# Kernel tuning notes

Hardware: AMD Instinct MI355X
Metric: run time of the kernel (lower is better)

## Reference

```python
import jax, jax.numpy as jnp
import numpy as np

D, H, E = 1024, 4096, 8


def setup_inputs() -> dict:
    key = jax.random.key(0)
    ks = jax.random.split(key, 8)
    s_in = 1.0 / np.sqrt(D)
    s_hid = 1.0 / np.sqrt(H)
    return {
        "x": jax.random.normal(ks[0], (4, 2048, D), dtype=jnp.float32),
        # torch nn.Linear init ~ U(-1/sqrt(fan_in), 1/sqrt(fan_in)); exact dist irrelevant for a numeric reference
        "Wg": jax.random.uniform(ks[1], (D, E), jnp.float32, -s_in, s_in),
        "bg": jax.random.uniform(ks[2], (E,), jnp.float32, -s_in, s_in),
        "W1": jax.random.uniform(ks[3], (E, D, H), jnp.float32, -s_in, s_in),
        "b1": jax.random.uniform(ks[4], (E, H), jnp.float32, -s_in, s_in),
        "W2": jax.random.uniform(ks[5], (E, H, D), jnp.float32, -s_hid, s_hid),
        "b2": jax.random.uniform(ks[6], (E, D), jnp.float32, -s_hid, s_hid),
    }


def reference(x, Wg, bg, W1, b1, W2, b2):
    # gate
    gate_logits = jnp.einsum("bsd,de->bse", x, Wg) + bg
    gate_probs = jax.nn.softmax(gate_logits, axis=-1)
    expert_indices = jnp.argmax(gate_probs, axis=-1)  # [B,S]

    # Faithful to source: mask the INPUT per expert, run the full MLP on the
    # masked input (biases still apply to zeroed tokens!), and sum all experts.
    onehot = jax.nn.one_hot(expert_indices, E, dtype=x.dtype)  # [B,S,E]
    xm = jnp.einsum("bsd,bse->ebsd", x, onehot)                # [E,B,S,D]
    h = jax.nn.relu(jnp.einsum("ebsd,edh->ebsh", xm, W1) + b1[:, None, None, :])
    out_e = jnp.einsum("ebsh,ehd->ebsd", h, W2) + b2[:, None, None, :]
    combined_output = jnp.sum(out_e, axis=0)                   # [B,S,D]
    return combined_output, gate_probs, expert_indices
```

## Files before the change

### kernel.cpp

```cpp
#include <hip/hip_runtime.h>
#include <hip/hip_bf16.h>
#include <cstdint>

#define D_DIM 1024
#define H_DIM 4096
#define E_NUM 8
#define NTOK  8192

#define BM 128
#define BN 128
#define BK 32

#define MAXT 72
#define NBY1 (H_DIM / BN)
#define NBY2 (D_DIM / BN)

typedef __bf16 bf16;
typedef __bf16 bf16x8 __attribute__((ext_vector_type(8)));
typedef __bf16 bf16x4 __attribute__((ext_vector_type(4)));
typedef float  f32x4  __attribute__((ext_vector_type(4)));

#define GLOAD16(g, l)                                                          \
    __builtin_amdgcn_global_load_lds(                                          \
        (const __attribute__((address_space(1))) void*)(g),                    \
        (__attribute__((address_space(3))) void*)(l), 16, 0, 0)

__global__ __launch_bounds__(256) void gate_kernel(
    const float* __restrict__ x, const float* __restrict__ Wg,
    const float* __restrict__ bg, float* __restrict__ out_probs,
    float* __restrict__ out_idx, int* __restrict__ cnt, int* __restrict__ list)
{
    const int t = blockIdx.x * 4 + (threadIdx.x >> 6);
    const int l = threadIdx.x & 63;
    double part[E_NUM];
#pragma unroll
    for (int e = 0; e < E_NUM; e++) part[e] = 0.0;
    const float* xr = x + (size_t)t * D_DIM;
#pragma unroll
    for (int i = 0; i < D_DIM / 64; i++) {
        const int d = l + i * 64;
        const float xv = xr[d];
        const float* wr = Wg + (size_t)d * E_NUM;
        float4 w0 = *(const float4*)(wr);
        float4 w1 = *(const float4*)(wr + 4);
        part[0] += (double)xv * (double)w0.x;
        part[1] += (double)xv * (double)w0.y;
        part[2] += (double)xv * (double)w0.z;
        part[3] += (double)xv * (double)w0.w;
        part[4] += (double)xv * (double)w1.x;
        part[5] += (double)xv * (double)w1.y;
        part[6] += (double)xv * (double)w1.z;
        part[7] += (double)xv * (double)w1.w;
    }
#pragma unroll
    for (int e = 0; e < E_NUM; e++) {
        double v = part[e];
        for (int s = 32; s > 0; s >>= 1) v += __shfl_xor(v, s, 64);
        part[e] = v;
    }
    if (l == 0) {
        float logits[E_NUM], probs[E_NUM];
        float m = -3.0e38f;
#pragma unroll
        for (int e = 0; e < E_NUM; e++) {
            logits[e] = (float)(part[e] + (double)bg[e]);
            m = fmaxf(m, logits[e]);
        }
        float s = 0.f;
#pragma unroll
        for (int e = 0; e < E_NUM; e++) { probs[e] = expf(logits[e] - m); s += probs[e]; }
        const float inv = 1.f / s;
        int best = 0; float bp = -1.f;
#pragma unroll
        for (int e = 0; e < E_NUM; e++) {
            probs[e] *= inv;
            if (probs[e] > bp) { bp = probs[e]; best = e; }
        }
#pragma unroll
        for (int e = 0; e < E_NUM; e++) out_probs[(size_t)t * E_NUM + e] = probs[e];
        out_idx[t] = (float)best;
        const int pos = atomicAdd(&cnt[best], 1);
        list[best * NTOK + pos] = t;
    }
}

__global__ __launch_bounds__(256) void zero_kernel(int* cnt, float* cpartial)
{
    const int i = blockIdx.x * 256 + threadIdx.x;
    if (i < E_NUM * D_DIM) cpartial[i] = 0.f;
    if (i < E_NUM) cnt[i] = 0;
}

__global__ void offsets_kernel(const int* __restrict__ cnt, int* __restrict__ off,
                               int* __restrict__ tile_e, int* __restrict__ tile_row,
                               int* __restrict__ tile_n)
{
    if (threadIdx.x == 0) {
        int a = 0, n = 0;
        for (int e = 0; e < E_NUM; e++) {
            off[e] = a; a += cnt[e];
            for (int rr = 0; rr < cnt[e]; rr += BM) {
                tile_e[n] = e; tile_row[n] = rr; n++;
            }
        }
        tile_n[0] = n;
    }
}

__global__ __launch_bounds__(256) void gather_kernel(
    const float* __restrict__ x, const int* __restrict__ off,
    const int* __restrict__ cnt, const int* __restrict__ list,
    bf16* __restrict__ Xg)
{
    const int p = blockIdx.x;
    int e = 0;
    while (e < E_NUM - 1 && p >= off[e] + cnt[e]) e++;
    const int token = list[e * NTOK + (p - off[e])];
    const float* src = x + (size_t)token * D_DIM;
    bf16* dst = Xg + (size_t)p * D_DIM;
    const int t = threadIdx.x;
    float4 v = *(const float4*)(src + t * 4);
    bf16x4 o;
    o[0] = (bf16)v.x; o[1] = (bf16)v.y; o[2] = (bf16)v.z; o[3] = (bf16)v.w;
    *(bf16x4*)(dst + t * 4) = o;
}

__global__ __launch_bounds__(256) void transpose_conv_kernel(
    const float* __restrict__ in, bf16* __restrict__ out, int K, int N)
{
    const int e = blockIdx.z;
    const float* src = in + (size_t)e * K * N;
    bf16* dst = out + (size_t)e * K * N;
    __shared__ float T[64][65];
    const int t = threadIdx.x;
    const int k0 = blockIdx.x * 64, n0 = blockIdx.y * 64;
    {
        const int ty = t >> 4;
        const int tx = (t & 15) * 4;
#pragma unroll
        for (int i = 0; i < 4; i++) {
            f32x4 v = __builtin_nontemporal_load(
                (const f32x4*)(src + (size_t)(k0 + ty + 16 * i) * N + n0 + tx));
            T[ty + 16 * i][tx + 0] = v[0]; T[ty + 16 * i][tx + 1] = v[1];
            T[ty + 16 * i][tx + 2] = v[2]; T[ty + 16 * i][tx + 3] = v[3];
        }
    }
    __syncthreads();
    {
        const int n  = t >> 2;
        const int kx = (t & 3) * 16;
        bf16 tmp[16];
#pragma unroll
        for (int j = 0; j < 16; j++) tmp[j] = (bf16)T[kx + j][n];
        *(bf16x8*)(dst + (size_t)(n0 + n) * K + k0 + kx)     = *(bf16x8*)&tmp[0];
        *(bf16x8*)(dst + (size_t)(n0 + n) * K + k0 + kx + 8) = *(bf16x8*)&tmp[8];
    }
}

__global__ __launch_bounds__(256) void transpose_conv_w2_kernel(
    const float* __restrict__ in, const float* __restrict__ b1,
    bf16* __restrict__ out, float* __restrict__ cpartial)
{
    const int K = H_DIM, N = D_DIM;
    const int e = blockIdx.z;
    const float* src = in + (size_t)e * K * N;
    bf16* dst = out + (size_t)e * K * N;
    __shared__ float T[64][65];
    const int t = threadIdx.x;
    const int k0 = blockIdx.x * 64, n0 = blockIdx.y * 64;
    {
        const int ty = t >> 4;
        const int tx = (t & 15) * 4;
#pragma unroll
        for (int i = 0; i < 4; i++) {
            f32x4 v = __builtin_nontemporal_load(
                (const f32x4*)(src + (size_t)(k0 + ty + 16 * i) * N + n0 + tx));
            T[ty + 16 * i][tx + 0] = v[0]; T[ty + 16 * i][tx + 1] = v[1];
            T[ty + 16 * i][tx + 2] = v[2]; T[ty + 16 * i][tx + 3] = v[3];
        }
    }
    __syncthreads();
    {
        const int n  = t >> 2;
        const int kx = (t & 3) * 16;
        bf16 tmp[16];
#pragma unroll
        for (int j = 0; j < 16; j++) tmp[j] = (bf16)T[kx + j][n];
        *(bf16x8*)(dst + (size_t)(n0 + n) * K + k0 + kx)     = *(bf16x8*)&tmp[0];
        *(bf16x8*)(dst + (size_t)(n0 + n) * K + k0 + kx + 8) = *(bf16x8*)&tmp[8];
    }
    if (t < 64) {
        float s = 0.f;
#pragma unroll 8
        for (int h = 0; h < 64; h++)
            s += fmaxf(b1[(size_t)e * H_DIM + k0 + h], 0.f) * T[h][t];
        atomicAdd(&cpartial[(size_t)e * D_DIM + n0 + t], s);
    }
}

__global__ __launch_bounds__(256) void cfinal_kernel(
    const float* __restrict__ cpartial, const float* __restrict__ b2,
    float* __restrict__ adj)
{
    const int d = blockIdx.x * 256 + threadIdx.x;
    float c[E_NUM];
    float tot = 0.f;
#pragma unroll
    for (int e = 0; e < E_NUM; e++) {
        c[e] = cpartial[(size_t)e * D_DIM + d] + b2[(size_t)e * D_DIM + d];
        tot += c[e];
    }
#pragma unroll
    for (int e = 0; e < E_NUM; e++) adj[(size_t)e * D_DIM + d] = tot - c[e];
}

__global__ __launch_bounds__(256) void gemm1_kernel(
    const bf16* __restrict__ Xg, const bf16* __restrict__ W1t,
    const float* __restrict__ b1, const int* __restrict__ cnt,
    const int* __restrict__ off, const int* __restrict__ tile_e,
    const int* __restrict__ tile_row, const int* __restrict__ tile_n,
    bf16* __restrict__ Hb)
{
    const int orig = blockIdx.x;
    const int q = (MAXT * NBY1) >> 3;
    const int fid = (orig & 7) * q + (orig >> 3);
    const int tx = fid % MAXT;
    const int by = fid / MAXT;
    if (tx >= tile_n[0]) return;
    const int e  = tile_e[tx];
    const int m0 = tile_row[tx];
    const int ne = cnt[e];
    const int oe = off[e];

    __shared__ bf16 As[BM * BK];
    __shared__ bf16 Bs[BN * BK];

    const int t = threadIdx.x;
    const int w = t >> 6, lane = t & 63;
    const int wr = w >> 1, wc = w & 1;
    const int lrow = lane & 15, kq = (lane >> 4) * 8;

    const int lr = lane >> 2;
    const int lc = (lane & 3) * 8;
    const bf16* Ast = Xg + ((size_t)(oe + m0 + w * 32 + lr)) * D_DIM + lc;
    const bf16* Bst = W1t + ((size_t)e * H_DIM + by * BN + w * 32 + lr) * D_DIM + lc;
    bf16* Alds = As + (w * 32) * BK;
    bf16* Blds = Bs + (w * 32) * BK;

    f32x4 acc[4][4];
#pragma unroll
    for (int m = 0; m < 4; m++)
#pragma unroll
        for (int n = 0; n < 4; n++) acc[m][n] = (f32x4){0.f, 0.f, 0.f, 0.f};

    for (int kt = 0; kt < D_DIM / BK; kt++) {
        const int kc = kt * BK;
        GLOAD16(Ast + kc,              Alds);
        GLOAD16(Ast + 16 * D_DIM + kc, Alds + 16 * BK);
        GLOAD16(Bst + kc,              Blds);
        GLOAD16(Bst + 16 * D_DIM + kc, Blds + 16 * BK);
        __syncthreads();

        bf16x8 af[4], bfr[4];
#pragma unroll
        for (int m = 0; m < 4; m++)
            af[m] = *(const bf16x8*)&As[(wr * 64 + m * 16 + lrow) * BK + kq];
#pragma unroll
        for (int n = 0; n < 4; n++)
            bfr[n] = *(const bf16x8*)&Bs[(wc * 64 + n * 16 + lrow) * BK + kq];
#pragma unroll
        for (int m = 0; m < 4; m++)
#pragma unroll
            for (int n = 0; n < 4; n++)
                acc[m][n] = __builtin_amdgcn_mfma_f32_16x16x32_bf16(af[m], bfr[n], acc[m][n], 0, 0, 0);
        __syncthreads();
    }

#pragma unroll
    for (int m = 0; m < 4; m++) {
        const int rb0 = m0 + wr * 64 + m * 16 + ((lane >> 4) << 2);
#pragma unroll
        for (int n = 0; n < 4; n++) {
            const int gcol = by * BN + wc * 64 + n * 16 + (lane & 15);
            const float bias = b1[(size_t)e * H_DIM + gcol];
#pragma unroll
            for (int r = 0; r < 4; r++) {
                const int grow = rb0 + r;
                if (grow < ne) {
                    float v = acc[m][n][r] + bias;
                    Hb[((size_t)(oe + grow)) * H_DIM + gcol] = (bf16)fmaxf(v, 0.f);
                }
            }
        }
    }
}

__global__ __launch_bounds__(256) void gemm2_kernel(
    const bf16* __restrict__ Hb, const bf16* __restrict__ W2t,
    const float* __restrict__ b2, const float* __restrict__ adj,
    const int* __restrict__ cnt, const int* __restrict__ off,
    const int* __restrict__ tile_e, const int* __restrict__ tile_row,
    const int* __restrict__ tile_n, const int* __restrict__ list,
    float* __restrict__ out)
{
    const int orig = blockIdx.x;
    const int q = (MAXT * NBY2) >> 3;
    const int fid = (orig & 7) * q + (orig >> 3);
    const int tx = fid % MAXT;
    const int by = fid / MAXT;
    if (tx >= tile_n[0]) return;
    const int e  = tile_e[tx];
    const int m0 = tile_row[tx];
    const int ne = cnt[e];
    const int oe = off[e];

    __shared__ bf16 As[BM * BK];
    __shared__ bf16 Bs[BN * BK];

    const int t = threadIdx.x;
    const int w = t >> 6, lane = t & 63;
    const int wr = w >> 1, wc = w & 1;
    const int lrow = lane & 15, kq = (lane >> 4) * 8;

    const int lr = lane >> 2;
    const int lc = (lane & 3) * 8;
    const bf16* Ast = Hb + ((size_t)(oe + m0 + w * 32 + lr)) * H_DIM + lc;
    const bf16* Bst = W2t + ((size_t)e * D_DIM + by * BN + w * 32 + lr) * H_DIM + lc;
    bf16* Alds = As + (w * 32) * BK;
    bf16* Blds = Bs + (w * 32) * BK;

    f32x4 acc[4][4];
#pragma unroll
    for (int m = 0; m < 4; m++)
#pragma unroll
        for (int n = 0; n < 4; n++) acc[m][n] = (f32x4){0.f, 0.f, 0.f, 0.f};

    for (int kt = 0; kt < H_DIM / BK; kt++) {
        const int kc = kt * BK;
        GLOAD16(Ast + kc,              Alds);
        GLOAD16(Ast + 16 * H_DIM + kc, Alds + 16 * BK);
        GLOAD16(Bst + kc,              Blds);
        GLOAD16(Bst + 16 * H_DIM + kc, Blds + 16 * BK);
        __syncthreads();

        bf16x8 af[4], bfr[4];
#pragma unroll
        for (int m = 0; m < 4; m++)
            af[m] = *(const bf16x8*)&As[(wr * 64 + m * 16 + lrow) * BK + kq];
#pragma unroll
        for (int n = 0; n < 4; n++)
            bfr[n] = *(const bf16x8*)&Bs[(wc * 64 + n * 16 + lrow) * BK + kq];
#pragma unroll
        for (int m = 0; m < 4; m++)
#pragma unroll
            for (int n = 0; n < 4; n++)
                acc[m][n] = __builtin_amdgcn_mfma_f32_16x16x32_bf16(af[m], bfr[n], acc[m][n], 0, 0, 0);
        __syncthreads();
    }

#pragma unroll
    for (int m = 0; m < 4; m++) {
        const int rb0 = m0 + wr * 64 + m * 16 + ((lane >> 4) << 2);
#pragma unroll
        for (int n = 0; n < 4; n++) {
            const int gcol = by * BN + wc * 64 + n * 16 + (lane & 15);
            const float badj = b2[(size_t)e * D_DIM + gcol] + adj[(size_t)e * D_DIM + gcol];
#pragma unroll
            for (int r = 0; r < 4; r++) {
                const int grow = rb0 + r;
                if (grow < ne) {
                    const int tok = list[e * NTOK + grow];
                    out[(size_t)tok * D_DIM + gcol] = acc[m][n][r] + badj;
                }
            }
        }
    }
}

extern "C" void kernel_launch(void* const* d_in, const int* in_sizes, int n_in,
                              void* d_out, int out_size, void* d_ws, size_t ws_size,
                              hipStream_t stream)
{
    (void)in_sizes; (void)n_in; (void)out_size; (void)ws_size;
    const float* x  = (const float*)d_in[0];
    const float* Wg = (const float*)d_in[1];
    const float* bg = (const float*)d_in[2];
    const float* W1 = (const float*)d_in[3];
    const float* b1 = (const float*)d_in[4];
    const float* W2 = (const float*)d_in[5];
    const float* b2 = (const float*)d_in[6];

    float* out_comb  = (float*)d_out;
    float* out_probs = out_comb + (size_t)NTOK * D_DIM;
    float* out_idx   = out_probs + (size_t)NTOK * E_NUM;

    char* ws = (char*)d_ws;
    size_t o = 0;
    bf16* W1t = (bf16*)(ws + o); o += (size_t)E_NUM * H_DIM * D_DIM * 2;
    bf16* W2t = (bf16*)(ws + o); o += (size_t)E_NUM * H_DIM * D_DIM * 2;
    bf16* Hb  = (bf16*)(ws + o); o += (size_t)NTOK * H_DIM * 2;
    bf16* Xg  = (bf16*)(ws + o); o += (size_t)NTOK * D_DIM * 2;
    float* cpartial = (float*)(ws + o); o += (size_t)E_NUM * D_DIM * 4;
    float* adj      = (float*)(ws + o); o += (size_t)E_NUM * D_DIM * 4;
    int* cnt  = (int*)(ws + o); o += 256;
    int* off  = (int*)(ws + o); o += 256;
    int* tile_e   = (int*)(ws + o); o += 512;
    int* tile_row = (int*)(ws + o); o += 512;
    int* tile_n   = (int*)(ws + o); o += 256;
    int* list = (int*)(ws + o); o += (size_t)E_NUM * NTOK * 4;

    zero_kernel<<<(E_NUM * D_DIM + 255) / 256, 256, 0, stream>>>(cnt, cpartial);
    gate_kernel<<<NTOK / 4, 256, 0, stream>>>(x, Wg, bg, out_probs, out_idx, cnt, list);
    offsets_kernel<<<1, 64, 0, stream>>>(cnt, off, tile_e, tile_row, tile_n);
    gather_kernel<<<NTOK, 256, 0, stream>>>(x, off, cnt, list, Xg);
    transpose_conv_w2_kernel<<<dim3(H_DIM / 64, D_DIM / 64, E_NUM), 256, 0, stream>>>(W2, b1, W2t, cpartial);
    cfinal_kernel<<<D_DIM / 256, 256, 0, stream>>>(cpartial, b2, adj);
    transpose_conv_kernel<<<dim3(D_DIM / 64, H_DIM / 64, E_NUM), 256, 0, stream>>>(W1, W1t, D_DIM, H_DIM);
    gemm1_kernel<<<MAXT * NBY1, 256, 0, stream>>>(Xg, W1t, b1, cnt, off, tile_e, tile_row, tile_n, Hb);
    gemm2_kernel<<<MAXT * NBY2, 256, 0, stream>>>(Hb, W2t, b2, adj, cnt, off, tile_e, tile_row, tile_n, list, out_comb);
}
```

Baseline: 441.1 us.

## Split-K the second expert GEMM and add a reduction kernel

```diff
diff --git a/kernel.cpp b/kernel.cpp
--- a/kernel.cpp
+++ b/kernel.cpp
@@ -14,6 +14,8 @@
 #define MAXT 72
 #define NBY1 (H_DIM / BN)
 #define NBY2 (D_DIM / BN)
+#define KSPLIT 2
+#define KC_LEN (H_DIM / KSPLIT)
 
 typedef __bf16 bf16;
 typedef __bf16 bf16x8 __attribute__((ext_vector_type(8)));
@@ -297,17 +299,17 @@
 
 __global__ __launch_bounds__(256) void gemm2_kernel(
     const bf16* __restrict__ Hb, const bf16* __restrict__ W2t,
-    const float* __restrict__ b2, const float* __restrict__ adj,
     const int* __restrict__ cnt, const int* __restrict__ off,
     const int* __restrict__ tile_e, const int* __restrict__ tile_row,
-    const int* __restrict__ tile_n, const int* __restrict__ list,
-    float* __restrict__ out)
+    const int* __restrict__ tile_n, float* __restrict__ part)
 {
     const int orig = blockIdx.x;
-    const int q = (MAXT * NBY2) >> 3;
+    const int q = (MAXT * NBY2 * KSPLIT) >> 3;
     const int fid = (orig & 7) * q + (orig >> 3);
     const int tx = fid % MAXT;
-    const int by = fid / MAXT;
+    const int byk = fid / MAXT;
+    const int by = byk >> 1;
+    const int kcs = byk & 1;
     if (tx >= tile_n[0]) return;
     const int e  = tile_e[tx];
     const int m0 = tile_row[tx];
@@ -324,8 +326,9 @@
 
     const int lr = lane >> 2;
     const int lc = (lane & 3) * 8;
-    const bf16* Ast = Hb + ((size_t)(oe + m0 + w * 32 + lr)) * H_DIM + lc;
-    const bf16* Bst = W2t + ((size_t)e * D_DIM + by * BN + w * 32 + lr) * H_DIM + lc;
+    const size_t kbase = (size_t)kcs * KC_LEN;
+    const bf16* Ast = Hb + ((size_t)(oe + m0 + w * 32 + lr)) * H_DIM + kbase + lc;
+    const bf16* Bst = W2t + ((size_t)e * D_DIM + by * BN + w * 32 + lr) * H_DIM + kbase + lc;
     bf16* Alds = As + (w * 32) * BK;
     bf16* Blds = Bs + (w * 32) * BK;
 
@@ -335,7 +338,7 @@
 #pragma unroll
         for (int n = 0; n < 4; n++) acc[m][n] = (f32x4){0.f, 0.f, 0.f, 0.f};
 
-    for (int kt = 0; kt < H_DIM / BK; kt++) {
+    for (int kt = 0; kt < KC_LEN / BK; kt++) {
         const int kc = kt * BK;
         GLOAD16(Ast + kc,              Alds);
         GLOAD16(Ast + 16 * H_DIM + kc, Alds + 16 * BK);
@@ -358,23 +361,40 @@
         __syncthreads();
     }
 
+    float* pdst = part + (size_t)kcs * NTOK * D_DIM;
 #pragma unroll
     for (int m = 0; m < 4; m++) {
         const int rb0 = m0 + wr * 64 + m * 16 + ((lane >> 4) << 2);
 #pragma unroll
         for (int n = 0; n < 4; n++) {
             const int gcol = by * BN + wc * 64 + n * 16 + (lane & 15);
-            const float badj = b2[(size_t)e * D_DIM + gcol] + adj[(size_t)e * D_DIM + gcol];
 #pragma unroll
             for (int r = 0; r < 4; r++) {
                 const int grow = rb0 + r;
-                if (grow < ne) {
-                    const int tok = list[e * NTOK + grow];
-                    out[(size_t)tok * D_DIM + gcol] = acc[m][n][r] + badj;
-                }
+                if (grow < ne)
+                    pdst[(size_t)(oe + grow) * D_DIM + gcol] = acc[m][n][r];
             }
         }
     }
+}
+
+__global__ __launch_bounds__(256) void reduce_kernel(
+    const float* __restrict__ part, const int* __restrict__ off,
+    const int* __restrict__ cnt, const int* __restrict__ list,
+    const float* __restrict__ b2, const float* __restrict__ adj,
+    float* __restrict__ out)
+{
+    const int p = blockIdx.x;
+    int e = 0;
+    while (e < E_NUM - 1 && p >= off[e] + cnt[e]) e++;
+    const int token = list[e * NTOK + (p - off[e])];
+    const int d = threadIdx.x * 4;
+    f32x4 a = *(const f32x4*)(part + (size_t)p * D_DIM + d);
+    f32x4 b = *(const f32x4*)(part + ((size_t)NTOK + p) * D_DIM + d);
+    f32x4 bb = *(const f32x4*)(b2 + (size_t)e * D_DIM + d);
+    f32x4 aj = *(const f32x4*)(adj + (size_t)e * D_DIM + d);
+    f32x4 r = a + b + bb + aj;
+    *(f32x4*)(out + (size_t)token * D_DIM + d) = r;
 }
 
 extern "C" void kernel_launch(void* const* d_in, const int* in_sizes, int n_in,
@@ -408,6 +428,7 @@
     int* tile_row = (int*)(ws + o); o += 512;
     int* tile_n   = (int*)(ws + o); o += 256;
     int* list = (int*)(ws + o); o += (size_t)E_NUM * NTOK * 4;
+    float* part = (float*)W1t;
 
     zero_kernel<<<(E_NUM * D_DIM + 255) / 256, 256, 0, stream>>>(cnt, cpartial);
     gate_kernel<<<NTOK / 4, 256, 0, stream>>>(x, Wg, bg, out_probs, out_idx, cnt, list);
@@ -417,5 +438,6 @@
     cfinal_kernel<<<D_DIM / 256, 256, 0, stream>>>(cpartial, b2, adj);
     transpose_conv_kernel<<<dim3(D_DIM / 64, H_DIM / 64, E_NUM), 256, 0, stream>>>(W1, W1t, D_DIM, H_DIM);
     gemm1_kernel<<<MAXT * NBY1, 256, 0, stream>>>(Xg, W1t, b1, cnt, off, tile_e, tile_row, tile_n, Hb);
-    gemm2_kernel<<<MAXT * NBY2, 256, 0, stream>>>(Hb, W2t, b2, adj, cnt, off, tile_e, tile_row, tile_n, list, out_comb);
-}
+    gemm2_kernel<<<MAXT * NBY2 * KSPLIT, 256, 0, stream>>>(Hb, W2t, cnt, off, tile_e, tile_row, tile_n, part);
+    reduce_kernel<<<NTOK, 256, 0, stream>>>(part, off, cnt, list, b2, adj, out_comb);
+}
```

Result: slower. 476.3 us (+8.0%).
